# Optimization experiments

Measured on AMD Instinct MI355X. Metric: run time of the kernel, lower is better.

The kernel has to match this reference:

```python
import jax, jax.numpy as jnp
import numpy as np
from math import factorial
from fractions import Fraction

# irreps: '0e + 1o + 2e + 3o' for in1, in2 and target (mul=1 each, channels separate)
L_IN1 = [0, 1, 2, 3]
L_IN2 = [0, 1, 2, 3]
L_MAX_OUT = 3
NCHANNELS = 64
BATCH = 10000
DIM_IN = sum(2 * l + 1 for l in L_IN1)  # 16


def _su2_cg(j1, m1, j2, m2, j3, m3):
    # Racah formula, exact rational arithmetic (matches e3nn _su2_cg)
    if m3 != m1 + m2 or not (abs(j1 - j2) <= j3 <= j1 + j2):
        return 0.0
    f = factorial
    vmin = max(-j1 + j2 + m3, -j1 + m1, 0)
    vmax = min(j2 + j3 + m1, j3 - j1 + j2, j3 + m3)
    C = (2 * j3 + 1) * Fraction(
        f(j3 + j1 - j2) * f(j3 - j1 + j2) * f(j1 + j2 - j3) * f(j3 + m3) * f(j3 - m3),
        f(j1 + j2 + j3 + 1) * f(j1 - m1) * f(j1 + m1) * f(j2 - m2) * f(j2 + m2))
    S = Fraction(0)
    for v in range(vmin, vmax + 1):
        S += (-1) ** (v + j2 + m2) * Fraction(
            f(j2 + j3 + m1 - v) * f(j1 - m1 + v),
            f(v) * f(j3 - j1 + j2 - v) * f(j3 + m3 - v) * f(v + j1 - j2 - m3))
    return float(C) ** 0.5 * float(S)


def _q_real_to_complex(l):
    # change of basis real SH -> complex SH (matches e3nn, incl. (-i)^l phase)
    q = np.zeros((2 * l + 1, 2 * l + 1), dtype=np.complex128)
    for m in range(-l, 0):
        q[l + m, l + abs(m)] = 1 / np.sqrt(2)
        q[l + m, l - abs(m)] = -1j / np.sqrt(2)
    q[l, l] = 1
    for m in range(1, l + 1):
        q[l + m, l + abs(m)] = (-1) ** m / np.sqrt(2)
        q[l + m, l - abs(m)] = 1j * (-1) ** m / np.sqrt(2)
    return (-1j) ** l * q


def _wigner_3j(l1, l2, l3):
    # real-basis Wigner 3j, unit Frobenius norm (matches e3nn o3.wigner_3j)
    C = np.zeros((2 * l1 + 1, 2 * l2 + 1, 2 * l3 + 1), dtype=np.complex128)
    for m1 in range(-l1, l1 + 1):
        for m2 in range(-l2, l2 + 1):
            for m3 in range(-l3, l3 + 1):
                C[l1 + m1, l2 + m2, l3 + m3] = _su2_cg(l1, m1, l2, m2, l3, m3)
    Q1, Q2, Q3 = _q_real_to_complex(l1), _q_real_to_complex(l2), _q_real_to_complex(l3)
    C = np.einsum('ij,kl,mn,ikn->jlm', Q1, Q2, np.conj(Q3.T), C)
    C = np.real(C)
    return C / np.linalg.norm(C)


def _build_sparse_cg():
    # enumerate instructions exactly as the torch module: i over in1, j over in2,
    # l3 ascending, kept iff parity matches target ((-1)^l3 == (-1)^(l1+l2)) and l3<=3.
    # component normalization, one path per output slot -> path_weight = sqrt(2*l3+1)
    mu1s, mu2s, mu3s, cgs = [], [], [], []
    off3 = 0
    for i, l1 in enumerate(L_IN1):
        off1 = sum(2 * l + 1 for l in L_IN1[:i])
        for j, l2 in enumerate(L_IN2):
            off2 = sum(2 * l + 1 for l in L_IN2[:j])
            for l3 in range(abs(l1 - l2), l1 + l2 + 1):
                if l3 > L_MAX_OUT or (l1 + l2 + l3) % 2 != 0:
                    continue
                cg = _wigner_3j(l1, l2, l3) * np.sqrt(2 * l3 + 1)
                m1, m2, m3 = np.nonzero(np.abs(cg) > 1e-12)
                mu1s.append(m1 + off1)
                mu2s.append(m2 + off2)
                mu3s.append(m3 + off3)
                cgs.append(cg[m1, m2, m3])
                off3 += 2 * l3 + 1
    return (np.concatenate(mu1s).astype(np.int32),
            np.concatenate(mu2s).astype(np.int32),
            np.concatenate(mu3s).astype(np.int32),
            np.concatenate(cgs).astype(np.float32),
            off3)


MU1, MU2, MU3, CG_NP, DIM_OUT = _build_sparse_cg()  # DIM_OUT == 99
CG = jnp.asarray(CG_NP)


def setup_inputs() -> dict:
    key = jax.random.key(0)
    k1, k2 = jax.random.split(key)
    x = jax.random.normal(k1, (BATCH, DIM_IN, NCHANNELS), dtype=jnp.float32)
    y = jax.random.normal(k2, (BATCH, DIM_IN, NCHANNELS), dtype=jnp.float32)
    return {"x": x, "y": y}


def reference(x, y):
    # fused gather-multiply-scatter over all CG nonzeros, vectorized over batch
    g = x[:, MU1, :] * CG[None, :, None] * y[:, MU2, :]  # [B, nnz, C]
    out = jnp.zeros((x.shape[0], DIM_OUT, x.shape[2]), x.dtype).at[:, MU3, :].add(g)
    return out
```

## Files before the change

### kernel.cpp

```cpp
#include <hip/hip_runtime.h>

#define BATCH 10000
#define NCH 64
#define DIM_IN 16
#define DIM_OUT 99

typedef float f32x4 __attribute__((ext_vector_type(4)));

namespace cgc {

struct cx { double re; double im; };

constexpr cx cmul(cx a, cx b) {
    return cx{a.re * b.re - a.im * b.im, a.re * b.im + a.im * b.re};
}

constexpr double cfact(int n) {
    double r = 1.0;
    for (int i = 2; i <= n; ++i) r *= (double)i;
    return r;
}

constexpr double csqrt(double x) {
    if (x <= 0.0) return 0.0;
    double y = x > 1.0 ? x : 1.0;
    for (int i = 0; i < 100; ++i) y = 0.5 * (y + x / y);
    return y;
}

constexpr int imax(int a, int b) { return a > b ? a : b; }
constexpr int imin(int a, int b) { return a < b ? a : b; }
constexpr int iabs(int a) { return a < 0 ? -a : a; }

constexpr double su2_cg(int j1, int m1, int j2, int m2, int j3, int m3) {
    if (m3 != m1 + m2) return 0.0;
    if (j3 < iabs(j1 - j2) || j3 > j1 + j2) return 0.0;
    int vmin = imax(imax(-j1 + j2 + m3, -j1 + m1), 0);
    int vmax = imin(imin(j2 + j3 + m1, j3 - j1 + j2), j3 + m3);
    double C = (2.0 * j3 + 1.0) *
        (cfact(j3 + j1 - j2) * cfact(j3 - j1 + j2) * cfact(j1 + j2 - j3) *
         cfact(j3 + m3) * cfact(j3 - m3)) /
        (cfact(j1 + j2 + j3 + 1) * cfact(j1 - m1) * cfact(j1 + m1) *
         cfact(j2 - m2) * cfact(j2 + m2));
    double S = 0.0;
    for (int v = vmin; v <= vmax; ++v) {
        double t = (cfact(j2 + j3 + m1 - v) * cfact(j1 - m1 + v)) /
                   (cfact(v) * cfact(j3 - j1 + j2 - v) * cfact(j3 + m3 - v) *
                    cfact(v + j1 - j2 - m3));
        S += ((v + j2 + m2) & 1) ? -t : t;
    }
    return csqrt(C) * S;
}

constexpr void fill_q(int l, cx* q) {
    const int n = 2 * l + 1;
    const double is2 = 0.70710678118654752440;
    for (int e = 0; e < n * n; ++e) q[e] = cx{0.0, 0.0};
    for (int m = -l; m < 0; ++m) {
        q[(l + m) * n + (l - m)] = cx{is2, 0.0};
        q[(l + m) * n + (l + m)] = cx{0.0, -is2};
    }
    q[l * n + l] = cx{1.0, 0.0};
    for (int m = 1; m <= l; ++m) {
        double s = (m & 1) ? -1.0 : 1.0;
        q[(l + m) * n + (l + m)] = cx{s * is2, 0.0};
        q[(l + m) * n + (l - m)] = cx{0.0, s * is2};
    }
    cx ph = (l & 3) == 0 ? cx{1.0, 0.0}
          : (l & 3) == 1 ? cx{0.0, -1.0}
          : (l & 3) == 2 ? cx{-1.0, 0.0}
                         : cx{0.0, 1.0};
    for (int e = 0; e < n * n; ++e) q[e] = cmul(ph, q[e]);
}

template<int l1, int l2, int l3>
struct InstCG { float v[(2 * l1 + 1) * (2 * l2 + 1) * (2 * l3 + 1)]; };

template<int l1, int l2, int l3>
constexpr InstCG<l1, l2, l3> make_inst() {
    constexpr int n1 = 2 * l1 + 1, n2 = 2 * l2 + 1, n3 = 2 * l3 + 1;
    double C[n1 * n2 * n3] = {};
    for (int i = 0; i < n1; ++i)
        for (int k = 0; k < n2; ++k)
            for (int nn = 0; nn < n3; ++nn)
                C[(i * n2 + k) * n3 + nn] = su2_cg(l1, i - l1, l2, k - l2, l3, nn - l3);
    cx Q1[n1 * n1] = {}; cx Q2[n2 * n2] = {}; cx Q3[n3 * n3] = {};
    fill_q(l1, Q1); fill_q(l2, Q2); fill_q(l3, Q3);
    double R[n1 * n2 * n3] = {};
    double ss = 0.0;
    for (int j = 0; j < n1; ++j)
        for (int lc = 0; lc < n2; ++lc)
            for (int m = 0; m < n3; ++m) {
                double ar = 0.0;
                for (int i = 0; i < n1; ++i) {
                    cx q1 = Q1[i * n1 + j];
                    if (q1.re == 0.0 && q1.im == 0.0) continue;
                    for (int k = 0; k < n2; ++k) {
                        cx q12 = cmul(q1, Q2[k * n2 + lc]);
                        if (q12.re == 0.0 && q12.im == 0.0) continue;
                        for (int nn = 0; nn < n3; ++nn) {
                            double cc = C[(i * n2 + k) * n3 + nn];
                            if (cc == 0.0) continue;
                            cx q3 = Q3[nn * n3 + m];
                            ar += (q12.re * q3.re + q12.im * q3.im) * cc;
                        }
                    }
                }
                R[(j * n2 + lc) * n3 + m] = ar;
                ss += ar * ar;
            }
    double scale = csqrt((double)n3) / csqrt(ss);
    InstCG<l1, l2, l3> T{};
    for (int e = 0; e < n1 * n2 * n3; ++e) T.v[e] = (float)(R[e] * scale);
    return T;
}

}

template<int l1, int l2, int l3, int o1, int o3>
__device__ __forceinline__ void do_inst(const f32x4* xv, const f32x4* ybl, f32x4* o4) {
    constexpr int n1 = 2 * l1 + 1, n2 = 2 * l2 + 1, n3 = 2 * l3 + 1;
    constexpr cgc::InstCG<l1, l2, l3> T = cgc::make_inst<l1, l2, l3>();
    f32x4 acc[n3];
#pragma unroll
    for (int m3 = 0; m3 < n3; ++m3) acc[m3] = (f32x4)0.0f;
#pragma unroll
    for (int m1 = 0; m1 < n1; ++m1) {
#pragma unroll
        for (int m2 = 0; m2 < n2; ++m2) {
            const f32x4 p = xv[o1 + m1] * ybl[m2];
#pragma unroll
            for (int m3 = 0; m3 < n3; ++m3) {
                const float c = T.v[(m1 * n2 + m2) * n3 + m3];
                if (c != 0.0f) acc[m3] += c * p;
            }
        }
    }
#pragma unroll
    for (int m3 = 0; m3 < n3; ++m3)
        o4[(o3 + m3) * 16] = acc[m3];
}

__global__ __launch_bounds__(64, 3) void tp_main(const float* __restrict__ x,
                                                 const float* __restrict__ y,
                                                 float* __restrict__ out) {
    const int g = blockIdx.x * blockDim.x + threadIdx.x;
    const int b = g >> 4;
    const int cl = g & 15;

    const f32x4* x4 = reinterpret_cast<const f32x4*>(x + (size_t)b * (DIM_IN * NCH)) + cl;
    const f32x4* y4 = reinterpret_cast<const f32x4*>(y + (size_t)b * (DIM_IN * NCH)) + cl;
    f32x4* o4 = reinterpret_cast<f32x4*>(out + (size_t)b * (DIM_OUT * NCH)) + cl;

    f32x4 xv[DIM_IN];
#pragma unroll
    for (int i = 0; i < DIM_IN; ++i) xv[i] = __builtin_nontemporal_load(&x4[i * 16]);

    {
        f32x4 ybl[1];
        ybl[0] = __builtin_nontemporal_load(&y4[0 * 16]);
        do_inst<0,0,0, 0,0 >(xv, ybl, o4);
        do_inst<1,0,1, 1,16>(xv, ybl, o4);
        do_inst<2,0,2, 4,40>(xv, ybl, o4);
        do_inst<3,0,3, 9,71>(xv, ybl, o4);
    }
    {
        f32x4 ybl[3];
#pragma unroll
        for (int k = 0; k < 3; ++k) ybl[k] = __builtin_nontemporal_load(&y4[(1 + k) * 16]);
        do_inst<0,1,1, 0,1 >(xv, ybl, o4);
        do_inst<1,1,0, 1,19>(xv, ybl, o4);
        do_inst<1,1,2, 1,20>(xv, ybl, o4);
        do_inst<2,1,1, 4,45>(xv, ybl, o4);
        do_inst<2,1,3, 4,48>(xv, ybl, o4);
        do_inst<3,1,2, 9,78>(xv, ybl, o4);
    }
    {
        f32x4 ybl[5];
#pragma unroll
        for (int k = 0; k < 5; ++k) ybl[k] = __builtin_nontemporal_load(&y4[(4 + k) * 16]);
        do_inst<0,2,2, 0,4 >(xv, ybl, o4);
        do_inst<1,2,1, 1,25>(xv, ybl, o4);
        do_inst<1,2,3, 1,28>(xv, ybl, o4);
        do_inst<2,2,0, 4,55>(xv, ybl, o4);
        do_inst<2,2,2, 4,56>(xv, ybl, o4);
        do_inst<3,2,1, 9,83>(xv, ybl, o4);
        do_inst<3,2,3, 9,86>(xv, ybl, o4);
    }
    {
        f32x4 ybl[7];
#pragma unroll
        for (int k = 0; k < 7; ++k) ybl[k] = __builtin_nontemporal_load(&y4[(9 + k) * 16]);
        do_inst<0,3,3, 0,9 >(xv, ybl, o4);
        do_inst<1,3,2, 1,35>(xv, ybl, o4);
        do_inst<2,3,1, 4,61>(xv, ybl, o4);
        do_inst<2,3,3, 4,64>(xv, ybl, o4);
        do_inst<3,3,0, 9,93>(xv, ybl, o4);
        do_inst<3,3,2, 9,94>(xv, ybl, o4);
    }
}

extern "C" void kernel_launch(void* const* d_in, const int* in_sizes, int n_in,
                              void* d_out, int out_size, void* d_ws, size_t ws_size,
                              hipStream_t stream) {
    const float* x = (const float*)d_in[0];
    const float* y = (const float*)d_in[1];
    float* out = (float*)d_out;
    hipLaunchKernelGGL(tp_main, dim3(BATCH * 16 / 64), dim3(64), 0, stream,
                       x, y, out);
}
```

Before: 67.94 us.

## Split tensor-product work across two blocks by input-1 parity

Doubles the grid so each pair of blocks handles the same batch/channel slice. One block computes the even-l1 instructions (l1=0,2) and the other the odd-l1 instructions (l1=1,3). Each block loads only the x components it needs, but y is now loaded twice. The intent is to cut per-thread register pressure and serial work, giving more occupancy and parallelism, at the cost of redundant y reads and an uneven split of work between the two halves.

```diff
diff --git a/kernel.cpp b/kernel.cpp
--- a/kernel.cpp
+++ b/kernel.cpp
@@ -117,8 +117,8 @@
 
 }
 
-template<int l1, int l2, int l3, int o1, int o3>
-__device__ __forceinline__ void do_inst(const f32x4* xv, const f32x4* ybl, f32x4* o4) {
+template<int l1, int l2, int l3, int o1l, int o3>
+__device__ __forceinline__ void do_inst(const f32x4* xl, const f32x4* ybl, f32x4* o4) {
     constexpr int n1 = 2 * l1 + 1, n2 = 2 * l2 + 1, n3 = 2 * l3 + 1;
     constexpr cgc::InstCG<l1, l2, l3> T = cgc::make_inst<l1, l2, l3>();
     f32x4 acc[n3];
@@ -128,7 +128,7 @@
     for (int m1 = 0; m1 < n1; ++m1) {
 #pragma unroll
         for (int m2 = 0; m2 < n2; ++m2) {
-            const f32x4 p = xv[o1 + m1] * ybl[m2];
+            const f32x4 p = xl[o1l + m1] * ybl[m2];
 #pragma unroll
             for (int m3 = 0; m3 < n3; ++m3) {
                 const float c = T.v[(m1 * n2 + m2) * n3 + m3];
@@ -144,7 +144,9 @@
 __global__ __launch_bounds__(64, 3) void tp_main(const float* __restrict__ x,
                                                  const float* __restrict__ y,
                                                  float* __restrict__ out) {
-    const int g = blockIdx.x * blockDim.x + threadIdx.x;
+    const int bid = blockIdx.x;
+    const int half = bid & 1;
+    const int g = (bid >> 1) * 64 + threadIdx.x;
     const int b = g >> 4;
     const int cl = g & 15;
 
@@ -152,51 +154,80 @@
     const f32x4* y4 = reinterpret_cast<const f32x4*>(y + (size_t)b * (DIM_IN * NCH)) + cl;
     f32x4* o4 = reinterpret_cast<f32x4*>(out + (size_t)b * (DIM_OUT * NCH)) + cl;
 
-    f32x4 xv[DIM_IN];
-#pragma unroll
-    for (int i = 0; i < DIM_IN; ++i) xv[i] = __builtin_nontemporal_load(&x4[i * 16]);
-
-    {
-        f32x4 ybl[1];
-        ybl[0] = __builtin_nontemporal_load(&y4[0 * 16]);
-        do_inst<0,0,0, 0,0 >(xv, ybl, o4);
-        do_inst<1,0,1, 1,16>(xv, ybl, o4);
-        do_inst<2,0,2, 4,40>(xv, ybl, o4);
-        do_inst<3,0,3, 9,71>(xv, ybl, o4);
-    }
-    {
-        f32x4 ybl[3];
-#pragma unroll
-        for (int k = 0; k < 3; ++k) ybl[k] = __builtin_nontemporal_load(&y4[(1 + k) * 16]);
-        do_inst<0,1,1, 0,1 >(xv, ybl, o4);
-        do_inst<1,1,0, 1,19>(xv, ybl, o4);
-        do_inst<1,1,2, 1,20>(xv, ybl, o4);
-        do_inst<2,1,1, 4,45>(xv, ybl, o4);
-        do_inst<2,1,3, 4,48>(xv, ybl, o4);
-        do_inst<3,1,2, 9,78>(xv, ybl, o4);
-    }
-    {
-        f32x4 ybl[5];
-#pragma unroll
-        for (int k = 0; k < 5; ++k) ybl[k] = __builtin_nontemporal_load(&y4[(4 + k) * 16]);
-        do_inst<0,2,2, 0,4 >(xv, ybl, o4);
-        do_inst<1,2,1, 1,25>(xv, ybl, o4);
-        do_inst<1,2,3, 1,28>(xv, ybl, o4);
-        do_inst<2,2,0, 4,55>(xv, ybl, o4);
-        do_inst<2,2,2, 4,56>(xv, ybl, o4);
-        do_inst<3,2,1, 9,83>(xv, ybl, o4);
-        do_inst<3,2,3, 9,86>(xv, ybl, o4);
-    }
-    {
-        f32x4 ybl[7];
-#pragma unroll
-        for (int k = 0; k < 7; ++k) ybl[k] = __builtin_nontemporal_load(&y4[(9 + k) * 16]);
-        do_inst<0,3,3, 0,9 >(xv, ybl, o4);
-        do_inst<1,3,2, 1,35>(xv, ybl, o4);
-        do_inst<2,3,1, 4,61>(xv, ybl, o4);
-        do_inst<2,3,3, 4,64>(xv, ybl, o4);
-        do_inst<3,3,0, 9,93>(xv, ybl, o4);
-        do_inst<3,3,2, 9,94>(xv, ybl, o4);
+    if (half == 0) {
+        f32x4 xl[6];
+        xl[0] = __builtin_nontemporal_load(&x4[0 * 16]);
+#pragma unroll
+        for (int k = 0; k < 5; ++k) xl[1 + k] = __builtin_nontemporal_load(&x4[(4 + k) * 16]);
+
+        {
+            f32x4 ybl[1];
+            ybl[0] = __builtin_nontemporal_load(&y4[0 * 16]);
+            do_inst<0,0,0, 0,0 >(xl, ybl, o4);
+            do_inst<2,0,2, 1,40>(xl, ybl, o4);
+        }
+        {
+            f32x4 ybl[3];
+#pragma unroll
+            for (int k = 0; k < 3; ++k) ybl[k] = __builtin_nontemporal_load(&y4[(1 + k) * 16]);
+            do_inst<0,1,1, 0,1 >(xl, ybl, o4);
+            do_inst<2,1,1, 1,45>(xl, ybl, o4);
+            do_inst<2,1,3, 1,48>(xl, ybl, o4);
+        }
+        {
+            f32x4 ybl[5];
+#pragma unroll
+            for (int k = 0; k < 5; ++k) ybl[k] = __builtin_nontemporal_load(&y4[(4 + k) * 16]);
+            do_inst<0,2,2, 0,4 >(xl, ybl, o4);
+            do_inst<2,2,0, 1,55>(xl, ybl, o4);
+            do_inst<2,2,2, 1,56>(xl, ybl, o4);
+        }
+        {
+            f32x4 ybl[7];
+#pragma unroll
+            for (int k = 0; k < 7; ++k) ybl[k] = __builtin_nontemporal_load(&y4[(9 + k) * 16]);
+            do_inst<0,3,3, 0,9 >(xl, ybl, o4);
+            do_inst<2,3,1, 1,61>(xl, ybl, o4);
+            do_inst<2,3,3, 1,64>(xl, ybl, o4);
+        }
+    } else {
+        f32x4 xl[10];
+#pragma unroll
+        for (int k = 0; k < 3; ++k) xl[k] = __builtin_nontemporal_load(&x4[(1 + k) * 16]);
+#pragma unroll
+        for (int k = 0; k < 7; ++k) xl[3 + k] = __builtin_nontemporal_load(&x4[(9 + k) * 16]);
+
+        {
+            f32x4 ybl[1];
+            ybl[0] = __builtin_nontemporal_load(&y4[0 * 16]);
+            do_inst<1,0,1, 0,16>(xl, ybl, o4);
+            do_inst<3,0,3, 3,71>(xl, ybl, o4);
+        }
+        {
+            f32x4 ybl[3];
+#pragma unroll
+            for (int k = 0; k < 3; ++k) ybl[k] = __builtin_nontemporal_load(&y4[(1 + k) * 16]);
+            do_inst<1,1,0, 0,19>(xl, ybl, o4);
+            do_inst<1,1,2, 0,20>(xl, ybl, o4);
+            do_inst<3,1,2, 3,78>(xl, ybl, o4);
+        }
+        {
+            f32x4 ybl[5];
+#pragma unroll
+            for (int k = 0; k < 5; ++k) ybl[k] = __builtin_nontemporal_load(&y4[(4 + k) * 16]);
+            do_inst<1,2,1, 0,25>(xl, ybl, o4);
+            do_inst<1,2,3, 0,28>(xl, ybl, o4);
+            do_inst<3,2,1, 3,83>(xl, ybl, o4);
+            do_inst<3,2,3, 3,86>(xl, ybl, o4);
+        }
+        {
+            f32x4 ybl[7];
+#pragma unroll
+            for (int k = 0; k < 7; ++k) ybl[k] = __builtin_nontemporal_load(&y4[(9 + k) * 16]);
+            do_inst<1,3,2, 0,35>(xl, ybl, o4);
+            do_inst<3,3,0, 3,93>(xl, ybl, o4);
+            do_inst<3,3,2, 3,94>(xl, ybl, o4);
+        }
     }
 }
 
@@ -206,6 +237,6 @@
     const float* x = (const float*)d_in[0];
     const float* y = (const float*)d_in[1];
     float* out = (float*)d_out;
-    hipLaunchKernelGGL(tp_main, dim3(BATCH * 16 / 64), dim3(64), 0, stream,
+    hipLaunchKernelGGL(tp_main, dim3(BATCH * 16 / 64 * 2), dim3(64), 0, stream,
                        x, y, out);
 }
```

After: 67.11 us. Within noise of the previous version (-1.2%).
